# Kernel tuning notes

Hardware: AMD Instinct MI355X
Metric: run time of the kernel (lower is better)

## Reference

```python
import jax, jax.numpy as jnp
import numpy as np

B, N, DM, H = 1, 2048, 1024, 16
CURV = 1.0  # hyperbolic curvature


def setup_inputs() -> dict:
    key = jax.random.key(0)
    ks = jax.random.split(key, 5)
    s = 1.0 / np.sqrt(DM)  # nn.Linear default init scale
    x = jax.random.normal(ks[0], (B, N, DM), dtype=jnp.float32)
    Wq = jax.random.uniform(ks[1], (DM, DM), jnp.float32, -s, s)
    Wk = jax.random.uniform(ks[2], (DM, DM), jnp.float32, -s, s)
    Wv = jax.random.uniform(ks[3], (DM, DM), jnp.float32, -s, s)
    Wo = jax.random.uniform(ks[4], (DM, DM), jnp.float32, -s, s)
    return {"x": x, "Wq": Wq, "Wk": Wk, "Wv": Wv, "Wo": Wo}


def reference(x, Wq, Wk, Wv, Wo):
    b, n, d = x.shape
    hd = d // H

    def split_heads(t):  # [B,N,D] -> [B,H,N,hd]
        return t.reshape(b, n, H, hd).transpose(0, 2, 1, 3)

    q = split_heads(x @ Wq.T)
    k = split_heads(x @ Wk.T)
    v = split_heads(x @ Wv.T)

    q_norm_sq = jnp.sum(q * q, axis=-1, keepdims=True)      # [B,H,N,1]
    k_norm_sq = jnp.sum(k * k, axis=-1)[:, :, None, :]      # [B,H,1,N]
    qk = jnp.einsum('bhnd,bhmd->bhnm', q, k)                # [B,H,N,N]

    diff_sq = jnp.maximum(q_norm_sq + k_norm_sq - 2.0 * qk, 0.0)
    denom = jnp.maximum((1.0 - CURV * q_norm_sq) * (1.0 - CURV * k_norm_sq), 1e-6)
    cosh_arg = jnp.maximum(1.0 + 2.0 * CURV * diff_sq / denom, 1.0)
    # safe acosh: acosh(1)=0; mask avoids inf grad at the boundary
    distance = jnp.where(cosh_arg > 1.0,
                         jnp.arccosh(jnp.maximum(cosh_arg, 1.0 + 1e-12)),
                         0.0)

    attn = jax.nn.softmax(-distance, axis=-1)               # [B,H,N,N]
    out = jnp.einsum('bhnm,bhmd->bhnd', attn, v)            # [B,H,N,hd]
    out = out.transpose(0, 2, 1, 3).reshape(b, n, d)
    return out @ Wo.T
```

## Files before the change

kernel.cpp:

```cpp
#include <hip/hip_runtime.h>
#include <math.h>

#define NSEQ   2048
#define DMODEL 1024
#define NHEADS 16
#define HD     64
#define NJH    2
#define JSPAN  (NSEQ / NJH)

typedef short bf16x8 __attribute__((ext_vector_type(8)));
typedef float f32x4  __attribute__((ext_vector_type(4)));
typedef unsigned short ushort8_t __attribute__((ext_vector_type(8)));

__device__ __forceinline__ unsigned short f2bf(float x) {
    unsigned int u = __builtin_bit_cast(unsigned int, x);
    unsigned int r = (u + 0x7FFFu + ((u >> 16) & 1u)) >> 16;
    return (unsigned short)r;
}

__global__ __launch_bounds__(256) void convert_inputs(
    const float* __restrict__ x,  const float* __restrict__ Wq,
    const float* __restrict__ Wk, const float* __restrict__ Wv,
    const float* __restrict__ Wo,
    unsigned short* __restrict__ xb, unsigned short* __restrict__ Wb,
    unsigned short* __restrict__ Wob)
{
    const size_t i8 = ((size_t)blockIdx.x * 256 + threadIdx.x) * 8;
    const float* src;
    unsigned short* dst;
    if (i8 < (2ull << 20)) {
        src = x + i8;  dst = xb + i8;
    } else if (i8 < (5ull << 20)) {
        const size_t o = i8 - (2ull << 20);
        const size_t s = o >> 20;
        src = (s == 0 ? Wq : (s == 1 ? Wk : Wv)) + (o & ((1u << 20) - 1));
        dst = Wb + o;
    } else {
        const size_t o = i8 - (5ull << 20);
        src = Wo + o;  dst = Wob + o;
    }
    const float4 v0 = *reinterpret_cast<const float4*>(src);
    const float4 v1 = *reinterpret_cast<const float4*>(src + 4);
    ushort8_t r;
    r[0] = f2bf(v0.x); r[1] = f2bf(v0.y); r[2] = f2bf(v0.z); r[3] = f2bf(v0.w);
    r[4] = f2bf(v1.x); r[5] = f2bf(v1.y); r[6] = f2bf(v1.z); r[7] = f2bf(v1.w);
    *reinterpret_cast<ushort8_t*>(dst) = r;
}

template <int QKV>
__global__ __launch_bounds__(256) void gemm_bt_bf16(
    const unsigned short* __restrict__ A, const unsigned short* __restrict__ B,
    float* __restrict__ C0,
    unsigned short* __restrict__ QbO, float2* __restrict__ qnc2O,
    unsigned short* __restrict__ KbO, float2* __restrict__ knckO,
    unsigned short* __restrict__ VtO)
{
    __shared__ unsigned short Ahs[128 * 64];
    __shared__ unsigned short Bhs[64 * 64];

    const int bm   = blockIdx.x * 128;
    const int bn   = blockIdx.y * 64;
    const int t    = threadIdx.x;
    const int wid  = t >> 6;
    const int lane = t & 63;
    const int g    = lane >> 4;
    const int r    = lane & 15;
    const int wm   = wid * 32;

    const int sel = QKV ? (bn >> 10) : 0;
    const int bnl = QKV ? (bn & 1023) : bn;

    f32x4 acc[2][4];
#pragma unroll
    for (int i = 0; i < 2; ++i)
#pragma unroll
        for (int j = 0; j < 4; ++j) acc[i][j] = (f32x4){0.f, 0.f, 0.f, 0.f};

    const int srowA = t >> 1;
    const int shalA = t & 1;
    const int srowB = t >> 2;
    const int squadB = t & 3;

    const unsigned short* Ag = &A[(size_t)(bm + srowA) * DMODEL + shalA * 32];
    const unsigned short* Bg = &B[(size_t)(bn + srowB) * DMODEL + squadB * 16];

    ushort8_t av[4], bv[2];
#pragma unroll
    for (int c = 0; c < 4; ++c)
        av[c] = *reinterpret_cast<const ushort8_t*>(Ag + c * 8);
#pragma unroll
    for (int c = 0; c < 2; ++c)
        bv[c] = *reinterpret_cast<const ushort8_t*>(Bg + c * 8);

    for (int k0 = 0; k0 < DMODEL; k0 += 64) {
        __syncthreads();
#pragma unroll
        for (int c = 0; c < 4; ++c) {
            const int sw = ((shalA * 4 + c) ^ (srowA & 7)) * 8;
            *reinterpret_cast<ushort8_t*>(&Ahs[srowA * 64 + sw]) = av[c];
        }
#pragma unroll
        for (int c = 0; c < 2; ++c) {
            const int sw = ((squadB * 2 + c) ^ (srowB & 7)) * 8;
            *reinterpret_cast<ushort8_t*>(&Bhs[srowB * 64 + sw]) = bv[c];
        }
        if (k0 + 64 < DMODEL) {
#pragma unroll
            for (int c = 0; c < 4; ++c)
                av[c] = *reinterpret_cast<const ushort8_t*>(
                    Ag + k0 + 64 + c * 8);
#pragma unroll
            for (int c = 0; c < 2; ++c)
                bv[c] = *reinterpret_cast<const ushort8_t*>(
                    Bg + k0 + 64 + c * 8);
        }
        __syncthreads();

#pragma unroll
        for (int dc = 0; dc < 2; ++dc) {
            bf16x8 af[2], bfr[4];
#pragma unroll
            for (int mt = 0; mt < 2; ++mt)
                af[mt] = *reinterpret_cast<const bf16x8*>(
                    &Ahs[(wm + mt * 16 + r) * 64 + ((dc * 4 + g) ^ (r & 7)) * 8]);
#pragma unroll
            for (int nt = 0; nt < 4; ++nt)
                bfr[nt] = *reinterpret_cast<const bf16x8*>(
                    &Bhs[(nt * 16 + r) * 64 + ((dc * 4 + g) ^ (r & 7)) * 8]);
#pragma unroll
            for (int mt = 0; mt < 2; ++mt)
#pragma unroll
                for (int nt = 0; nt < 4; ++nt)
                    acc[mt][nt] = __builtin_amdgcn_mfma_f32_16x16x32_bf16(
                        af[mt], bfr[nt], acc[mt][nt], 0, 0, 0);
        }
    }

    if (QKV) {
        if (sel < 2) {
            unsigned short* Hb = sel ? KbO : QbO;
            float2* dst2 = sel ? knckO : qnc2O;
            const int hh = bnl >> 6;
#pragma unroll
            for (int mt = 0; mt < 2; ++mt) {
#pragma unroll
                for (int rg = 0; rg < 4; ++rg) {
                    float ss = 0.f;
#pragma unroll
                    for (int nt = 0; nt < 4; ++nt) {
                        const float v = acc[mt][nt][rg];
                        ss = fmaf(v, v, ss);
                        Hb[(size_t)(bm + wm + mt * 16 + g * 4 + rg) * 1024 +
                           bnl + nt * 16 + r] = f2bf(v);
                    }
                    ss += __shfl_xor(ss, 1, 64);
                    ss += __shfl_xor(ss, 2, 64);
                    ss += __shfl_xor(ss, 4, 64);
                    ss += __shfl_xor(ss, 8, 64);
                    if (r == 0) {
                        const int row = bm + wm + mt * 16 + g * 4 + rg;
                        dst2[hh * NSEQ + row] =
                            make_float2(ss, (sel ? 1.0f : 2.0f) / (1.0f - ss));
                    }
                }
            }
        } else {
#pragma unroll
            for (int mt = 0; mt < 2; ++mt)
#pragma unroll
                for (int nt = 0; nt < 4; ++nt) {
                    ushort4 o4;
                    o4.x = f2bf(acc[mt][nt][0]);
                    o4.y = f2bf(acc[mt][nt][1]);
                    o4.z = f2bf(acc[mt][nt][2]);
                    o4.w = f2bf(acc[mt][nt][3]);
                    *reinterpret_cast<ushort4*>(
                        &VtO[(size_t)(bnl + nt * 16 + r) * NSEQ +
                             bm + wm + mt * 16 + g * 4]) = o4;
                }
        }
    } else {
#pragma unroll
        for (int mt = 0; mt < 2; ++mt)
#pragma unroll
            for (int nt = 0; nt < 4; ++nt)
#pragma unroll
                for (int rg = 0; rg < 4; ++rg)
                    C0[(size_t)(bm + wm + mt * 16 + g * 4 + rg) * 1024 +
                       bnl + nt * 16 + r] = acc[mt][nt][rg];
    }
}

__global__ __launch_bounds__(256) void hyp_attn_v8(
    const unsigned short* __restrict__ Qb, const unsigned short* __restrict__ Kb,
    const unsigned short* __restrict__ Vt,
    const float2* __restrict__ qnc2_a, const float2* __restrict__ knck_a,
    float* __restrict__ Opart, float* __restrict__ lpart)
{
    __shared__ unsigned short Khs[64 * 64];
    __shared__ unsigned short Vts[64 * 64];
    __shared__ unsigned short Ps[4][16 * 64];
    __shared__ float2 kcs[JSPAN];

    const int h    = blockIdx.y;
    const int n0   = blockIdx.x * 64;
    const int jh   = blockIdx.z;
    const int t    = threadIdx.x;
    const int wid  = t >> 6;
    const int lane = t & 63;
    const int g    = lane >> 4;
    const int r    = lane & 15;
    const int qb   = n0 + wid * 16;

    bf16x8 qf[2];
#pragma unroll
    for (int dc = 0; dc < 2; ++dc)
        qf[dc] = *reinterpret_cast<const bf16x8*>(
            Qb + (size_t)(qb + r) * DMODEL + h * HD + dc * 32 + g * 8);

    float qn_r[4], c2q[4];
#pragma unroll
    for (int rg = 0; rg < 4; ++rg) {
        const float2 qv = qnc2_a[h * NSEQ + qb + g * 4 + rg];
        qn_r[rg] = qv.x;
        c2q[rg]  = qv.y;
    }
#pragma unroll
    for (int i = 0; i < JSPAN / 256; ++i)
        kcs[i * 256 + t] = knck_a[h * NSEQ + jh * JSPAN + i * 256 + t];

    f32x4 oacc[4];
#pragma unroll
    for (int nt = 0; nt < 4; ++nt) oacc[nt] = (f32x4){0.f, 0.f, 0.f, 0.f};
    float l_acc[4] = {0.f, 0.f, 0.f, 0.f};

    const int srow = t >> 2;
    const int c0   = (t & 3) * 2;
    const int sw0  = (c0 ^ (srow & 7)) * 8;
    const int sw1  = ((c0 + 1) ^ (srow & 7)) * 8;
    const int sg   = (t & 3) * 16;
    unsigned short* Pw = &Ps[wid][0];

    const unsigned short* Kg = Kb + (size_t)(jh * JSPAN + srow) * DMODEL + h * HD + sg;
    const unsigned short* Vg = Vt + (size_t)(h * HD + srow) * NSEQ + jh * JSPAN + sg;

    ushort8_t kr0 = *reinterpret_cast<const ushort8_t*>(Kg);
    ushort8_t kr1 = *reinterpret_cast<const ushort8_t*>(Kg + 8);
    ushort8_t vr0 = *reinterpret_cast<const ushort8_t*>(Vg);
    ushort8_t vr1 = *reinterpret_cast<const ushort8_t*>(Vg + 8);

    const int ntb = JSPAN / 64;
    for (int tb = 0; tb < ntb; ++tb) {
        __syncthreads();
        *reinterpret_cast<ushort8_t*>(&Khs[srow * 64 + sw0]) = kr0;
        *reinterpret_cast<ushort8_t*>(&Khs[srow * 64 + sw1]) = kr1;
        *reinterpret_cast<ushort8_t*>(&Vts[srow * 64 + sw0]) = vr0;
        *reinterpret_cast<ushort8_t*>(&Vts[srow * 64 + sw1]) = vr1;
        if (tb + 1 < ntb) {
            const unsigned short* kn_ = Kg + (size_t)(tb + 1) * 64 * DMODEL;
            const unsigned short* vn_ = Vg + (tb + 1) * 64;
            kr0 = *reinterpret_cast<const ushort8_t*>(kn_);
            kr1 = *reinterpret_cast<const ushort8_t*>(kn_ + 8);
            vr0 = *reinterpret_cast<const ushort8_t*>(vn_);
            vr1 = *reinterpret_cast<const ushort8_t*>(vn_ + 8);
        }
        __syncthreads();

#pragma unroll
        for (int jt = 0; jt < 4; ++jt) {
            f32x4 sac = (f32x4){0.f, 0.f, 0.f, 0.f};
#pragma unroll
            for (int dc = 0; dc < 2; ++dc) {
                const bf16x8 kb = *reinterpret_cast<const bf16x8*>(
                    &Khs[(jt * 16 + r) * 64 + ((dc * 4 + g) ^ (r & 7)) * 8]);
                sac = __builtin_amdgcn_mfma_f32_16x16x32_bf16(qf[dc], kb, sac, 0, 0, 0);
            }
            const float2 kc = kcs[tb * 64 + jt * 16 + r];
#pragma unroll
            for (int rg = 0; rg < 4; ++rg) {
                const float dsq = fmaf(-2.f, sac[rg], qn_r[rg] + kc.x);
                const float ca  = fmaxf(fmaf(dsq, c2q[rg] * kc.y, 1.f), 1.0f);
                const float s2  = fmaf(ca, ca, -1.f);
                const float wj  = ca - __builtin_amdgcn_sqrtf(s2);
                l_acc[rg] += wj;
                const int qrow = g * 4 + rg;
                Pw[qrow * 64 +
                   ((2 * jt + (r >> 3)) ^ (qrow & 7)) * 8 + (r & 7)] = f2bf(wj);
            }
        }

#pragma unroll
        for (int kc2 = 0; kc2 < 2; ++kc2) {
            const bf16x8 pa = *reinterpret_cast<const bf16x8*>(
                &Pw[r * 64 + ((kc2 * 4 + g) ^ (r & 7)) * 8]);
#pragma unroll
            for (int nt = 0; nt < 4; ++nt) {
                const bf16x8 vb = *reinterpret_cast<const bf16x8*>(
                    &Vts[(nt * 16 + r) * 64 + ((kc2 * 4 + g) ^ (r & 7)) * 8]);
                oacc[nt] = __builtin_amdgcn_mfma_f32_16x16x32_bf16(pa, vb, oacc[nt], 0, 0, 0);
            }
        }
    }

#pragma unroll
    for (int rg = 0; rg < 4; ++rg) {
        l_acc[rg] += __shfl_xor(l_acc[rg], 1, 64);
        l_acc[rg] += __shfl_xor(l_acc[rg], 2, 64);
        l_acc[rg] += __shfl_xor(l_acc[rg], 4, 64);
        l_acc[rg] += __shfl_xor(l_acc[rg], 8, 64);
    }

    float* Op = Opart + (size_t)jh * NSEQ * DMODEL;
#pragma unroll
    for (int nt = 0; nt < 4; ++nt)
#pragma unroll
        for (int rg = 0; rg < 4; ++rg)
            Op[(size_t)(qb + g * 4 + rg) * DMODEL + h * HD + nt * 16 + r] =
                oacc[nt][rg];
    if (r == 0) {
#pragma unroll
        for (int rg = 0; rg < 4; ++rg)
            lpart[(jh * NHEADS + h) * NSEQ + qb + g * 4 + rg] = l_acc[rg];
    }
}

__global__ __launch_bounds__(256) void merge_kernel(
    const float* __restrict__ Opart, const float* __restrict__ lpart,
    unsigned short* __restrict__ Ob)
{
    const size_t i8 = ((size_t)blockIdx.x * 256 + threadIdx.x) * 8;
    if (i8 >= (size_t)NSEQ * DMODEL) return;
    const int n  = (int)(i8 >> 10);
    const int dm = (int)(i8 & 1023);
    const int h  = dm >> 6;
    const float li = 1.0f / (lpart[h * NSEQ + n] +
                             lpart[(NHEADS + h) * NSEQ + n]);
    const float* O0 = Opart + i8;
    const float* O1 = Opart + (size_t)NSEQ * DMODEL + i8;
    ushort8_t o;
#pragma unroll
    for (int c = 0; c < 2; ++c) {
        const float4 a = *reinterpret_cast<const float4*>(O0 + c * 4);
        const float4 b = *reinterpret_cast<const float4*>(O1 + c * 4);
        o[c * 4 + 0] = f2bf((a.x + b.x) * li);
        o[c * 4 + 1] = f2bf((a.y + b.y) * li);
        o[c * 4 + 2] = f2bf((a.z + b.z) * li);
        o[c * 4 + 3] = f2bf((a.w + b.w) * li);
    }
    *reinterpret_cast<ushort8_t*>(Ob + i8) = o;
}

extern "C" void kernel_launch(void* const* d_in, const int* in_sizes, int n_in,
                              void* d_out, int out_size, void* d_ws, size_t ws_size,
                              hipStream_t stream)
{
    const float* x  = (const float*)d_in[0];
    const float* Wq = (const float*)d_in[1];
    const float* Wk = (const float*)d_in[2];
    const float* Wv = (const float*)d_in[3];
    const float* Wo = (const float*)d_in[4];
    float* out = (float*)d_out;

    char* ws = (char*)d_ws;
    const size_t MB = 1048576;
    unsigned short* xb   = (unsigned short*)(ws);
    unsigned short* Wb   = (unsigned short*)(ws + 4  * MB);
    unsigned short* Wob  = (unsigned short*)(ws + 10 * MB);
    unsigned short* Qbuf = (unsigned short*)(ws + 12 * MB);
    unsigned short* Kbuf = (unsigned short*)(ws + 16 * MB);
    unsigned short* Vt   = (unsigned short*)(ws + 20 * MB);
    float2*         qnc2 = (float2*)(ws + 24 * MB);
    float2*         knck = (float2*)(ws + 24 * MB + 262144);
    float*          Opart= (float*)(ws + 25 * MB);
    float*          lpart= (float*)(ws + 41 * MB);
    unsigned short* Ob   = xb;

    const dim3 blk(256);

    convert_inputs<<<3072, blk, 0, stream>>>(x, Wq, Wk, Wv, Wo, xb, Wb, Wob);

    gemm_bt_bf16<1><<<dim3(NSEQ / 128, 3072 / 64), blk, 0, stream>>>(
        xb, Wb, nullptr, Qbuf, qnc2, Kbuf, knck, Vt);

    hyp_attn_v8<<<dim3(NSEQ / 64, NHEADS, NJH), blk, 0, stream>>>(
        Qbuf, Kbuf, Vt, qnc2, knck, Opart, lpart);

    merge_kernel<<<(NSEQ * DMODEL / 8 + 255) / 256, blk, 0, stream>>>(
        Opart, lpart, Ob);

    gemm_bt_bf16<0><<<dim3(NSEQ / 128, DMODEL / 64), blk, 0, stream>>>(
        Ob, Wob, out, nullptr, nullptr, nullptr, nullptr, nullptr);
}
```

Before: 92.07 us.

## Drop key-split in hyperbolic attention and fuse normalization into epilogue

The attention kernel now processes the full key sequence per block instead of splitting keys across two blocks. It normalizes by the row sum and writes bf16 output directly. This removes the merge kernel and the fp32 partial-output round trip through global memory, at the cost of halving grid parallelism and doubling per-block loop length.

```diff
diff --git a/kernel.cpp b/kernel.cpp
--- a/kernel.cpp
+++ b/kernel.cpp
@@ -5,8 +5,6 @@
 #define DMODEL 1024
 #define NHEADS 16
 #define HD     64
-#define NJH    2
-#define JSPAN  (NSEQ / NJH)
 
 typedef short bf16x8 __attribute__((ext_vector_type(8)));
 typedef float f32x4  __attribute__((ext_vector_type(4)));
@@ -191,20 +189,19 @@
     }
 }
 
-__global__ __launch_bounds__(256) void hyp_attn_v8(
+__global__ __launch_bounds__(256) void hyp_attn_v9(
     const unsigned short* __restrict__ Qb, const unsigned short* __restrict__ Kb,
     const unsigned short* __restrict__ Vt,
     const float2* __restrict__ qnc2_a, const float2* __restrict__ knck_a,
-    float* __restrict__ Opart, float* __restrict__ lpart)
+    unsigned short* __restrict__ Ob)
 {
     __shared__ unsigned short Khs[64 * 64];
     __shared__ unsigned short Vts[64 * 64];
     __shared__ unsigned short Ps[4][16 * 64];
-    __shared__ float2 kcs[JSPAN];
+    __shared__ float2 kcs[NSEQ];
 
     const int h    = blockIdx.y;
     const int n0   = blockIdx.x * 64;
-    const int jh   = blockIdx.z;
     const int t    = threadIdx.x;
     const int wid  = t >> 6;
     const int lane = t & 63;
@@ -226,8 +223,8 @@
         c2q[rg]  = qv.y;
     }
 #pragma unroll
-    for (int i = 0; i < JSPAN / 256; ++i)
-        kcs[i * 256 + t] = knck_a[h * NSEQ + jh * JSPAN + i * 256 + t];
+    for (int i = 0; i < NSEQ / 256; ++i)
+        kcs[i * 256 + t] = knck_a[h * NSEQ + i * 256 + t];
 
     f32x4 oacc[4];
 #pragma unroll
@@ -241,15 +238,15 @@
     const int sg   = (t & 3) * 16;
     unsigned short* Pw = &Ps[wid][0];
 
-    const unsigned short* Kg = Kb + (size_t)(jh * JSPAN + srow) * DMODEL + h * HD + sg;
-    const unsigned short* Vg = Vt + (size_t)(h * HD + srow) * NSEQ + jh * JSPAN + sg;
+    const unsigned short* Kg = Kb + (size_t)srow * DMODEL + h * HD + sg;
+    const unsigned short* Vg = Vt + (size_t)(h * HD + srow) * NSEQ + sg;
 
     ushort8_t kr0 = *reinterpret_cast<const ushort8_t*>(Kg);
     ushort8_t kr1 = *reinterpret_cast<const ushort8_t*>(Kg + 8);
     ushort8_t vr0 = *reinterpret_cast<const ushort8_t*>(Vg);
     ushort8_t vr1 = *reinterpret_cast<const ushort8_t*>(Vg + 8);
 
-    const int ntb = JSPAN / 64;
+    const int ntb = NSEQ / 64;
     for (int tb = 0; tb < ntb; ++tb) {
         __syncthreads();
         *reinterpret_cast<ushort8_t*>(&Khs[srow * 64 + sw0]) = kr0;
@@ -310,44 +307,15 @@
         l_acc[rg] += __shfl_xor(l_acc[rg], 8, 64);
     }
 
-    float* Op = Opart + (size_t)jh * NSEQ * DMODEL;
-#pragma unroll
-    for (int nt = 0; nt < 4; ++nt)
-#pragma unroll
-        for (int rg = 0; rg < 4; ++rg)
-            Op[(size_t)(qb + g * 4 + rg) * DMODEL + h * HD + nt * 16 + r] =
-                oacc[nt][rg];
-    if (r == 0) {
-#pragma unroll
-        for (int rg = 0; rg < 4; ++rg)
-            lpart[(jh * NHEADS + h) * NSEQ + qb + g * 4 + rg] = l_acc[rg];
-    }
-}
-
-__global__ __launch_bounds__(256) void merge_kernel(
-    const float* __restrict__ Opart, const float* __restrict__ lpart,
-    unsigned short* __restrict__ Ob)
-{
-    const size_t i8 = ((size_t)blockIdx.x * 256 + threadIdx.x) * 8;
-    if (i8 >= (size_t)NSEQ * DMODEL) return;
-    const int n  = (int)(i8 >> 10);
-    const int dm = (int)(i8 & 1023);
-    const int h  = dm >> 6;
-    const float li = 1.0f / (lpart[h * NSEQ + n] +
-                             lpart[(NHEADS + h) * NSEQ + n]);
-    const float* O0 = Opart + i8;
-    const float* O1 = Opart + (size_t)NSEQ * DMODEL + i8;
-    ushort8_t o;
-#pragma unroll
-    for (int c = 0; c < 2; ++c) {
-        const float4 a = *reinterpret_cast<const float4*>(O0 + c * 4);
-        const float4 b = *reinterpret_cast<const float4*>(O1 + c * 4);
-        o[c * 4 + 0] = f2bf((a.x + b.x) * li);
-        o[c * 4 + 1] = f2bf((a.y + b.y) * li);
-        o[c * 4 + 2] = f2bf((a.z + b.z) * li);
-        o[c * 4 + 3] = f2bf((a.w + b.w) * li);
-    }
-    *reinterpret_cast<ushort8_t*>(Ob + i8) = o;
+#pragma unroll
+    for (int rg = 0; rg < 4; ++rg) {
+        const float inv = 1.0f / l_acc[rg];
+        unsigned short* dst =
+            Ob + (size_t)(qb + g * 4 + rg) * DMODEL + h * HD + r;
+#pragma unroll
+        for (int nt = 0; nt < 4; ++nt)
+            dst[nt * 16] = f2bf(oacc[nt][rg] * inv);
+    }
 }
 
 extern "C" void kernel_launch(void* const* d_in, const int* in_sizes, int n_in,
@@ -371,8 +339,6 @@
     unsigned short* Vt   = (unsigned short*)(ws + 20 * MB);
     float2*         qnc2 = (float2*)(ws + 24 * MB);
     float2*         knck = (float2*)(ws + 24 * MB + 262144);
-    float*          Opart= (float*)(ws + 25 * MB);
-    float*          lpart= (float*)(ws + 41 * MB);
     unsigned short* Ob   = xb;
 
     const dim3 blk(256);
@@ -382,11 +348,8 @@
     gemm_bt_bf16<1><<<dim3(NSEQ / 128, 3072 / 64), blk, 0, stream>>>(
         xb, Wb, nullptr, Qbuf, qnc2, Kbuf, knck, Vt);
 
-    hyp_attn_v8<<<dim3(NSEQ / 64, NHEADS, NJH), blk, 0, stream>>>(
-        Qbuf, Kbuf, Vt, qnc2, knck, Opart, lpart);
-
-    merge_kernel<<<(NSEQ * DMODEL / 8 + 255) / 256, blk, 0, stream>>>(
-        Opart, lpart, Ob);
+    hyp_attn_v9<<<dim3(NSEQ / 64, NHEADS), blk, 0, stream>>>(
+        Qbuf, Kbuf, Vt, qnc2, knck, Ob);
 
     gemm_bt_bf16<0><<<dim3(NSEQ / 128, DMODEL / 64), blk, 0, stream>>>(
         Ob, Wob, out, nullptr, nullptr, nullptr, nullptr, nullptr);
```

Result: slower. 94.70 us (+2.9%).
